# Performance work log

Measured on AMD Instinct MI355X. Metric: run time of the kernel, lower is better.

Reference implementation:

```python
import jax, jax.numpy as jnp
import numpy as np
from jax.ops import segment_sum

N = 100000
E = 3200000
IN_DIM = 256
OUT_DIM = 64
LN_EPS = 1e-5
NEG_SLOPE = 0.01


def setup_inputs() -> dict:
    key = jax.random.key(0)
    k1, k2, k3, k4, k5 = jax.random.split(key, 5)
    x = jax.random.normal(k1, (N, IN_DIM), dtype=jnp.float32)
    edge_index = jax.random.randint(k2, (2, E), 0, N, dtype=jnp.int32)
    edge_weight = jax.random.uniform(k3, (E,), dtype=jnp.float32)
    # GCNConv params (glorot-ish scale) + LayerNorm params
    W = jax.random.normal(k4, (IN_DIM, OUT_DIM), dtype=jnp.float32) / np.sqrt(IN_DIM)
    b = jnp.zeros((OUT_DIM,), dtype=jnp.float32)
    gamma = jnp.ones((OUT_DIM,), dtype=jnp.float32)
    beta = jnp.zeros((OUT_DIM,), dtype=jnp.float32)
    return {"x": x, "edge_index": edge_index, "edge_weight": edge_weight,
            "W": W, "b": b, "gamma": gamma, "beta": beta}


def _gcn_forward(x, edge_index, edge_weight, W, b, gamma, beta):
    n = x.shape[0]
    # add self-loops with weight 1 (PyG GCNConv default)
    loops = jnp.arange(n, dtype=edge_index.dtype)
    src = jnp.concatenate([edge_index[0], loops])   # [E+N] message sources
    dst = jnp.concatenate([edge_index[1], loops])   # [E+N] aggregation targets
    ew = jnp.concatenate([edge_weight, jnp.ones((n,), dtype=edge_weight.dtype)])
    # symmetric normalization: deg computed on dst via weighted scatter
    deg = segment_sum(ew, dst, num_segments=n)                   # [N]
    dinv = jnp.where(deg > 0, jax.lax.rsqrt(deg), 0.0)           # deg^{-1/2}
    norm = dinv[src] * ew * dinv[dst]                            # [E+N]
    h = x @ W                                                    # [N, OUT]
    agg = segment_sum(h[src] * norm[:, None], dst, num_segments=n)  # [N, OUT]
    y = agg + b
    # leaky_relu then LayerNorm over last dim
    y = jnp.where(y >= 0, y, NEG_SLOPE * y)
    mu = jnp.mean(y, axis=-1, keepdims=True)
    var = jnp.mean(jnp.square(y - mu), axis=-1, keepdims=True)
    return (y - mu) * jax.lax.rsqrt(var + LN_EPS) * gamma + beta


def reference(x, edge_index, edge_weight, W, b, gamma, beta):
    return _gcn_forward(x, edge_index, edge_weight, W, b, gamma, beta)
```

## Files before the change

### kernel.cpp

```cpp
#include <hip/hip_runtime.h>

#define NN 100000
#define NE 3200000
#define OVCAP 65536

#define BINSZ 64
#define NBIN ((NN + BINSZ - 1) / BINSZ)
#define NSEG 8
#define BINPAD 16
#define MAXPB 4096

struct OvEnt { int dst; int src; float ew; int pad; };


__global__ void k_zero(int* __restrict__ bincnt, int* __restrict__ ovcnt, int n) {
    int i = blockIdx.x * 256 + threadIdx.x;
    if (i < n) bincnt[i] = 0;
    if (i == 0) *ovcnt = 0;
}

__global__ void k_binscatter(const int* __restrict__ src, const int* __restrict__ dst,
                             const float* __restrict__ ew, int* __restrict__ bincnt,
                             uint2* __restrict__ binbuf, int segcap,
                             OvEnt* __restrict__ ov, int* __restrict__ ovcnt, int e) {
    int i = blockIdx.x * 256 + threadIdx.x;
    int seg = blockIdx.x & (NSEG - 1);
    if (i >= e) return;
    int s = src[i], d = dst[i];
    float w = ew[i];
    int cell = (d >> 6) * NSEG + seg;
    int pos = atomicAdd(&bincnt[cell * BINPAD], 1);
    if (pos < segcap) {
        unsigned key = (unsigned)s | ((unsigned)(d & 63) << 17);
        binbuf[(size_t)cell * segcap + pos] = make_uint2(key, __float_as_uint(w));
    } else {
        int op = atomicAdd(ovcnt, 1);
        if (op < OVCAP) { OvEnt t; t.dst = d; t.src = s; t.ew = w; t.pad = 0; ov[op] = t; }
    }
}

__global__ __launch_bounds__(256) void k_binsort(
    const int* __restrict__ bincnt, uint2* __restrict__ binbuf, int segcap,
    const OvEnt* __restrict__ ov, const int* __restrict__ ovcnt,
    float* __restrict__ dinv, int* __restrict__ off, int* __restrict__ ncnt,
    int* __restrict__ binov, int n) {
    __shared__ float sdeg[BINSZ];
    __shared__ int hcnt[BINSZ];
    __shared__ int hoff[BINSZ];
    __shared__ int spref[NSEG + 1];
    __shared__ int sov;
    __shared__ uint2 sbuf[MAXPB];
    int bin = blockIdx.x, t = threadIdx.x;
    if (t < BINSZ) { sdeg[t] = 0.f; hcnt[t] = 0; }
    if (t == 0) {
        int pref = 0, anyov = 0;
        for (int s2 = 0; s2 < NSEG; s2++) {
            int c = bincnt[(bin * NSEG + s2) * BINPAD];
            spref[s2] = pref;
            pref += (c < segcap ? c : segcap);
            if (c > segcap) anyov = 1;
        }
        spref[NSEG] = pref;
        sov = anyov;
        binov[bin] = anyov;
    }
    __syncthreads();
    int bc = spref[NSEG];
    uint2* base = binbuf + (size_t)bin * NSEG * segcap;
    for (int s2 = 0; s2 < NSEG; s2++) {
        int beg = spref[s2], len = spref[s2 + 1] - beg;
        const uint2* sp = base + (size_t)s2 * segcap;
        for (int j = t; j < len; j += 256) sbuf[beg + j] = sp[j];
    }
    __syncthreads();
    uint2 ent[16];
    int ne = 0;
#pragma unroll
    for (int p = 0; p < 16; p++) {
        int idx = t + p * 256;
        if (idx < bc) { ent[p] = sbuf[idx]; ne = p + 1; }
    }
#pragma unroll
    for (int p = 0; p < 16; p++) {
        if (p < ne) {
            int dl = (int)((ent[p].x >> 17) & 63u);
            atomicAdd(&hcnt[dl], 1);
            atomicAdd(&sdeg[dl], __uint_as_float(ent[p].y));
        }
    }
    if (sov) {
        int on = *ovcnt; if (on > OVCAP) on = OVCAP;
        for (int j = t; j < on; j += 256) {
            OvEnt e2 = ov[j];
            if ((e2.dst >> 6) == bin) atomicAdd(&sdeg[e2.dst & 63], e2.ew);
        }
    }
    __syncthreads();
    if (t < 64) {
        int v = hcnt[t];
        int inc = v;
#pragma unroll
        for (int o2 = 1; o2 < 64; o2 <<= 1) {
            int u = __shfl_up(inc, o2, 64);
            if (t >= o2) inc += u;
        }
        int excl = inc - v;
        hoff[t] = excl;
        int g = bin * BINSZ + t;
        if (g < n) {
            dinv[g] = rsqrtf(1.0f + sdeg[t]);
            off[g] = bin * NSEG * segcap + excl;
            ncnt[g] = v;
        }
    }
    __syncthreads();
#pragma unroll
    for (int p = 0; p < 16; p++) {
        if (p < ne) {
            int dl = (int)((ent[p].x >> 17) & 63u);
            int pos = atomicAdd(&hoff[dl], 1);
            sbuf[pos] = ent[p];
        }
    }
    __syncthreads();
    for (int j = t; j < bc; j += 256) base[j] = sbuf[j];
}

__global__ __launch_bounds__(256) void k_gather_s(
    const float* __restrict__ h, const float* __restrict__ dinv,
    const int* __restrict__ binov,
    const int* __restrict__ off, const int* __restrict__ ncnt,
    const uint2* __restrict__ sorted,
    const OvEnt* __restrict__ ov, const int* __restrict__ ovcnt,
    const float* __restrict__ bias, const float* __restrict__ gamma,
    const float* __restrict__ beta, float* __restrict__ out, int n) {
    int lane = threadIdx.x & 63, wid = threadIdx.x >> 6;
    int node = blockIdx.x * 4 + wid;
    if (node >= n) return;
    float di = dinv[node];
    float acc = h[(size_t)node * 64 + lane] * di * di;
    int beg = off[node], c0 = ncnt[node];
    for (int j = 0; j < c0; j += 64) {
        int c = c0 - j; if (c > 64) c = 64;
        int s = 0; float w = 0.f;
        if (lane < c) {
            uint2 v = sorted[beg + j + lane];
            s = (int)(v.x & 0x1FFFFu);
            w = __uint_as_float(v.y) * dinv[s] * di;
        }
        int i2 = 0;
        for (; i2 + 16 <= c; i2 += 16) {
            float hv[16], wv[16];
#pragma unroll
            for (int q = 0; q < 16; q++) {
                int si = __shfl(s, i2 + q, 64);
                wv[q] = __shfl(w, i2 + q, 64);
                hv[q] = h[(size_t)si * 64 + lane];
            }
#pragma unroll
            for (int q = 0; q < 16; q++) acc += hv[q] * wv[q];
        }
        if (i2 < c) {
            float hv[16], wv[16];
            int rem = c - i2;
#pragma unroll
            for (int q = 0; q < 16; q++) {
                if (q < rem) {
                    int si = __shfl(s, i2 + q, 64);
                    wv[q] = __shfl(w, i2 + q, 64);
                    hv[q] = h[(size_t)si * 64 + lane];
                } else { wv[q] = 0.f; hv[q] = 0.f; }
            }
#pragma unroll
            for (int q = 0; q < 16; q++) acc += hv[q] * wv[q];
        }
    }
    if (binov[node >> 6]) {
        int on = *ovcnt; if (on > OVCAP) on = OVCAP;
        for (int j = 0; j < on; j++) {
            OvEnt ent = ov[j];
            if (ent.dst == node)
                acc += h[(size_t)ent.src * 64 + lane] * dinv[ent.src] * ent.ew * di;
        }
    }
    float y = acc + bias[lane];
    y = (y >= 0.f) ? y : 0.01f * y;
    float sum = y;
#pragma unroll
    for (int o = 32; o > 0; o >>= 1) sum += __shfl_xor(sum, o, 64);
    float mu = sum * (1.0f / 64.0f);
    float d = y - mu;
    float v = d * d;
#pragma unroll
    for (int o = 32; o > 0; o >>= 1) v += __shfl_xor(v, o, 64);
    v *= (1.0f / 64.0f);
    out[(size_t)node * 64 + lane] = d * rsqrtf(v + 1e-5f) * gamma[lane] + beta[lane];
}

#define GR 64
#define GKC 32
#define XS_STRIDE 36
__global__ __launch_bounds__(256) void k_gemm(const float* __restrict__ x,
                                              const float* __restrict__ W,
                                              float* __restrict__ h, int n) {
    __shared__ float xs[GR][XS_STRIDE];
    __shared__ float wsh[GKC][64];
    int t = threadIdx.x;
    int tx = t & 15;
    int ty = t >> 4;
    int rbase = blockIdx.x * GR;
    float acc[4][4];
#pragma unroll
    for (int i = 0; i < 4; i++)
#pragma unroll
        for (int j = 0; j < 4; j++) acc[i][j] = 0.0f;

    for (int k0 = 0; k0 < 256; k0 += GKC) {
        const float4* wsrc = (const float4*)(W + k0 * 64);
        float4* wdst = (float4*)(&wsh[0][0]);
        wdst[t] = wsrc[t];
        wdst[t + 256] = wsrc[t + 256];
#pragma unroll
        for (int p = 0; p < 2; p++) {
            int f4 = p * 256 + t;
            int r = f4 >> 3;
            int kq = (f4 & 7) << 2;
            int row = rbase + r;
            float4 val = make_float4(0.f, 0.f, 0.f, 0.f);
            if (row < n) val = *(const float4*)(x + (size_t)row * 256 + k0 + kq);
            *(float4*)(&xs[r][kq]) = val;
        }
        __syncthreads();
        int r0 = ty * 4, c0 = tx * 4;
#pragma unroll
        for (int kk = 0; kk < GKC; kk += 4) {
            float4 wv[4];
#pragma unroll
            for (int m = 0; m < 4; m++) wv[m] = *(const float4*)(&wsh[kk + m][c0]);
#pragma unroll
            for (int i = 0; i < 4; i++) {
                float4 xv = *(const float4*)(&xs[r0 + i][kk]);
                acc[i][0] += xv.x * wv[0].x + xv.y * wv[1].x + xv.z * wv[2].x + xv.w * wv[3].x;
                acc[i][1] += xv.x * wv[0].y + xv.y * wv[1].y + xv.z * wv[2].y + xv.w * wv[3].y;
                acc[i][2] += xv.x * wv[0].z + xv.y * wv[1].z + xv.z * wv[2].z + xv.w * wv[3].z;
                acc[i][3] += xv.x * wv[0].w + xv.y * wv[1].w + xv.z * wv[2].w + xv.w * wv[3].w;
            }
        }
        __syncthreads();
    }
    int r0 = ty * 4, c0 = tx * 4;
#pragma unroll
    for (int i = 0; i < 4; i++) {
        int row = rbase + r0 + i;
        if (row < n) {
            float4 v = make_float4(acc[i][0], acc[i][1], acc[i][2], acc[i][3]);
            *(float4*)(h + (size_t)row * 64 + c0) = v;
        }
    }
}


__global__ void k_init(float* __restrict__ deg, int* __restrict__ cnt, int n) {
    int i = blockIdx.x * 256 + threadIdx.x;
    if (i < n) { deg[i] = 1.0f; cnt[i] = 0; }
}

__global__ void k_deg(const int* __restrict__ dst, const float* __restrict__ ew,
                      float* __restrict__ deg, int* __restrict__ cnt, int e) {
    int i = blockIdx.x * 256 + threadIdx.x;
    if (i < e) {
        int d = dst[i];
        atomicAdd(&deg[d], ew[i]);
        atomicAdd(&cnt[d], 1);
    }
}

#define SCAN_T 256
#define SCAN_E 8
__global__ void k_scan_blocks(const int* __restrict__ cnt, int* __restrict__ off,
                              int* __restrict__ bsum, int n) {
    __shared__ int sdata[SCAN_T];
    int base = blockIdx.x * (SCAN_T * SCAN_E);
    int t = threadIdx.x;
    int v[SCAN_E];
    int local = 0;
    int idx0 = base + t * SCAN_E;
#pragma unroll
    for (int i = 0; i < SCAN_E; i++) {
        int idx = idx0 + i;
        int c = (idx < n) ? cnt[idx] : 0;
        v[i] = local;
        local += c;
    }
    sdata[t] = local;
    __syncthreads();
    for (int o = 1; o < SCAN_T; o <<= 1) {
        int x = 0;
        if (t >= o) x = sdata[t - o];
        __syncthreads();
        sdata[t] += x;
        __syncthreads();
    }
    int excl = sdata[t] - local;
#pragma unroll
    for (int i = 0; i < SCAN_E; i++) {
        int idx = idx0 + i;
        if (idx < n) off[idx] = excl + v[i];
    }
    if (t == SCAN_T - 1) bsum[blockIdx.x] = sdata[t];
}

__global__ void k_scan_bsums(int* __restrict__ bsum, int nb) {
    int t = threadIdx.x;
    int v = (t < nb) ? bsum[t] : 0;
    int orig = v;
#pragma unroll
    for (int o = 1; o < 64; o <<= 1) {
        int u = __shfl_up(v, o, 64);
        if (t >= o) v += u;
    }
    if (t < nb) bsum[t] = v - orig;
}

__global__ void k_finalize(int* __restrict__ off, const int* __restrict__ bsum,
                           int* __restrict__ cursor, float* __restrict__ deg,
                           int n, int total) {
    int i = blockIdx.x * 256 + threadIdx.x;
    if (i < n) {
        int o = off[i] + bsum[i >> 11];
        off[i] = o;
        cursor[i] = o;
        deg[i] = rsqrtf(deg[i]);
    }
    if (i == 0) off[n] = total;
}

__global__ void k_scatter(const int* __restrict__ src, const int* __restrict__ dst,
                          const float* __restrict__ ew, const float* __restrict__ dinv,
                          int* __restrict__ cursor, int* __restrict__ ssrc,
                          float* __restrict__ snorm, int e) {
    int i = blockIdx.x * 256 + threadIdx.x;
    if (i < e) {
        int s = src[i], d = dst[i];
        float nm = dinv[s] * ew[i] * dinv[d];
        int pos = atomicAdd(&cursor[d], 1);
        ssrc[pos] = s;
        snorm[pos] = nm;
    }
}

__global__ __launch_bounds__(256) void k_gather(
    const float* __restrict__ h, const float* __restrict__ dinv,
    const int* __restrict__ off, const int* __restrict__ ssrc,
    const float* __restrict__ snorm, const float* __restrict__ bias,
    const float* __restrict__ gamma, const float* __restrict__ beta,
    float* __restrict__ out, int n) {
    int lane = threadIdx.x & 63;
    int wid = threadIdx.x >> 6;
    int node = blockIdx.x * 4 + wid;
    if (node >= n) return;
    float di = dinv[node];
    float acc = h[(size_t)node * 64 + lane] * di * di;
    int beg = off[node], end = off[node + 1];
    for (int j = beg; j < end; j += 64) {
        int cnt = end - j;
        if (cnt > 64) cnt = 64;
        int s = 0;
        float w = 0.f;
        if (lane < cnt) { s = ssrc[j + lane]; w = snorm[j + lane]; }
        for (int i2 = 0; i2 < cnt; i2++) {
            int si = __shfl(s, i2, 64);
            float wi = __shfl(w, i2, 64);
            acc += h[(size_t)si * 64 + lane] * wi;
        }
    }
    float y = acc + bias[lane];
    y = (y >= 0.f) ? y : 0.01f * y;
    float sum = y;
#pragma unroll
    for (int o = 32; o > 0; o >>= 1) sum += __shfl_xor(sum, o, 64);
    float mu = sum * (1.0f / 64.0f);
    float d = y - mu;
    float v = d * d;
#pragma unroll
    for (int o = 32; o > 0; o >>= 1) v += __shfl_xor(v, o, 64);
    v *= (1.0f / 64.0f);
    out[(size_t)node * 64 + lane] = d * rsqrtf(v + 1e-5f) * gamma[lane] + beta[lane];
}


extern "C" void kernel_launch(void* const* d_in, const int* in_sizes, int n_in,
                              void* d_out, int out_size, void* d_ws, size_t ws_size,
                              hipStream_t stream) {
    const float* x = (const float*)d_in[0];
    const int* ei = (const int*)d_in[1];
    const float* ew = (const float*)d_in[2];
    const float* W = (const float*)d_in[3];
    const float* b = (const float*)d_in[4];
    const float* gamma = (const float*)d_in[5];
    const float* beta = (const float*)d_in[6];
    float* out = (float*)d_out;

    const int n = NN, e = NE;
    const int* src = ei;
    const int* dst = ei + e;

    char* ws = (char*)d_ws;
    size_t o = 0;
    auto alloc = [&](size_t bytes) -> char* {
        char* r = ws + o;
        o = (o + bytes + 255) & ~(size_t)255;
        return r;
    };
    auto pad = [](size_t bytes) -> size_t { return (bytes + 255) & ~(size_t)255; };

    int nb_n = (n + 255) / 256;
    int nb_e = (e + 255) / 256;
    int nb_gemm = (n + GR - 1) / GR;
    int nb_w = (n + 3) / 4;

    size_t fixed = 0;
    fixed += pad((size_t)NBIN * NSEG * BINPAD * 4);
    fixed += 256;
    fixed += pad((size_t)OVCAP * 16);
    fixed += pad((size_t)n * 4);
    fixed += pad((size_t)n * 4);
    fixed += pad((size_t)n * 4);
    fixed += pad((size_t)NBIN * 4);
    fixed += pad((size_t)n * 64 * 4);

    int segcap = 0;
    if (ws_size >= fixed + pad((size_t)NBIN * NSEG * 512 * 8) + 1024) segcap = 512;
    else if (ws_size >= fixed + pad((size_t)NBIN * NSEG * 384 * 8) + 1024) segcap = 384;

    if (segcap > 0) {
        int* bincnt = (int*)alloc((size_t)NBIN * NSEG * BINPAD * 4);
        int* ovcnt = (int*)alloc(4);
        OvEnt* ov = (OvEnt*)alloc((size_t)OVCAP * 16);
        float* dinv = (float*)alloc((size_t)n * 4);
        int* off = (int*)alloc((size_t)n * 4);
        int* ncnt = (int*)alloc((size_t)n * 4);
        int* binov = (int*)alloc((size_t)NBIN * 4);
        float* h = (float*)alloc((size_t)n * 64 * 4);
        uint2* binbuf = (uint2*)alloc((size_t)NBIN * NSEG * segcap * 8);

        int nz = NBIN * NSEG * BINPAD;
        int nb_z = (nz + 255) / 256;
        k_zero<<<nb_z, 256, 0, stream>>>(bincnt, ovcnt, nz);
        k_binscatter<<<nb_e, 256, 0, stream>>>(src, dst, ew, bincnt, binbuf, segcap,
                                               ov, ovcnt, e);
        k_binsort<<<NBIN, 256, 0, stream>>>(bincnt, binbuf, segcap, ov, ovcnt,
                                            dinv, off, ncnt, binov, n);
        k_gemm<<<nb_gemm, 256, 0, stream>>>(x, W, h, n);
        k_gather_s<<<nb_w, 256, 0, stream>>>(h, dinv, binov, off, ncnt, binbuf,
                                             ov, ovcnt, b, gamma, beta, out, n);
    } else {
        float* deg = (float*)alloc((size_t)n * 4);
        int* cnt = (int*)alloc((size_t)n * 4);
        int* off = (int*)alloc((size_t)(n + 1) * 4);
        int* cursor = (int*)alloc((size_t)n * 4);
        int* bsum = (int*)alloc(64 * 4);
        float* h = (float*)alloc((size_t)n * 64 * 4);
        int* ssrc = (int*)alloc((size_t)e * 4);
        float* snorm = (float*)alloc((size_t)e * 4);
        int nb_scan = (n + SCAN_T * SCAN_E - 1) / (SCAN_T * SCAN_E);

        k_init<<<nb_n, 256, 0, stream>>>(deg, cnt, n);
        k_deg<<<nb_e, 256, 0, stream>>>(dst, ew, deg, cnt, e);
        k_scan_blocks<<<nb_scan, SCAN_T, 0, stream>>>(cnt, off, bsum, n);
        k_scan_bsums<<<1, 64, 0, stream>>>(bsum, nb_scan);
        k_finalize<<<nb_n, 256, 0, stream>>>(off, bsum, cursor, deg, n, e);
        k_scatter<<<nb_e, 256, 0, stream>>>(src, dst, ew, deg, cursor, ssrc, snorm, e);
        k_gemm<<<nb_gemm, 256, 0, stream>>>(x, W, h, n);
        k_gather<<<nb_w, 256, 0, stream>>>(h, deg, off, ssrc, snorm, b, gamma, beta, out, n);
    }
}
```

Measured before the change: 515.8 us.

## Replace per-edge global atomics with block-local histogram reservation in bin scatter

The scatter kernel now processes a contiguous chunk of edges per block, builds a shared-memory histogram over destination bins, and reserves space in each bin with one global atomic per bin per block. Edges then get their slots through shared atomics, which removes the per-edge global atomic and the 8-way segment split. The sort kernel reads a single contiguous bin region directly from global memory instead of gathering segments through LDS. In exchange each block reads the edge arrays twice and touches all ~1563 bin counters, and a contiguous bin buffer of 4096 slots per bin is assumed.

```diff
diff --git a/kernel.cpp b/kernel.cpp
--- a/kernel.cpp
+++ b/kernel.cpp
@@ -6,9 +6,8 @@
 
 #define BINSZ 64
 #define NBIN ((NN + BINSZ - 1) / BINSZ)
-#define NSEG 8
-#define BINPAD 16
 #define MAXPB 4096
+#define SCAT_BLOCKS 512
 
 struct OvEnt { int dst; int src; float ew; int pad; };
 
@@ -19,66 +18,68 @@
     if (i == 0) *ovcnt = 0;
 }
 
-__global__ void k_binscatter(const int* __restrict__ src, const int* __restrict__ dst,
-                             const float* __restrict__ ew, int* __restrict__ bincnt,
-                             uint2* __restrict__ binbuf, int segcap,
-                             OvEnt* __restrict__ ov, int* __restrict__ ovcnt, int e) {
-    int i = blockIdx.x * 256 + threadIdx.x;
-    int seg = blockIdx.x & (NSEG - 1);
-    if (i >= e) return;
-    int s = src[i], d = dst[i];
-    float w = ew[i];
-    int cell = (d >> 6) * NSEG + seg;
-    int pos = atomicAdd(&bincnt[cell * BINPAD], 1);
-    if (pos < segcap) {
-        unsigned key = (unsigned)s | ((unsigned)(d & 63) << 17);
-        binbuf[(size_t)cell * segcap + pos] = make_uint2(key, __float_as_uint(w));
-    } else {
-        int op = atomicAdd(ovcnt, 1);
-        if (op < OVCAP) { OvEnt t; t.dst = d; t.src = s; t.ew = w; t.pad = 0; ov[op] = t; }
+__global__ __launch_bounds__(256) void k_binscatter(
+    const int* __restrict__ src, const int* __restrict__ dst,
+    const float* __restrict__ ew, int* __restrict__ bincnt,
+    uint2* __restrict__ binbuf, int cap,
+    OvEnt* __restrict__ ov, int* __restrict__ ovcnt, int e) {
+    __shared__ int hist[NBIN];
+    int t = threadIdx.x;
+    int chunk = (e + gridDim.x - 1) / gridDim.x;
+    int beg = blockIdx.x * chunk;
+    int end = beg + chunk; if (end > e) end = e;
+    for (int j = t; j < NBIN; j += 256) hist[j] = 0;
+    __syncthreads();
+    for (int i = beg + t; i < end; i += 256)
+        atomicAdd(&hist[dst[i] >> 6], 1);
+    __syncthreads();
+    for (int j = t; j < NBIN; j += 256) {
+        int c = hist[j];
+        hist[j] = (c > 0) ? atomicAdd(&bincnt[j], c) : 0;
+    }
+    __syncthreads();
+    for (int i = beg + t; i < end; i += 256) {
+        int s = src[i], d = dst[i];
+        float w = ew[i];
+        int bin = d >> 6;
+        int pos = atomicAdd(&hist[bin], 1);
+        if (pos < cap) {
+            unsigned key = (unsigned)s | ((unsigned)(d & 63) << 17);
+            binbuf[(size_t)bin * cap + pos] = make_uint2(key, __float_as_uint(w));
+        } else {
+            int op = atomicAdd(ovcnt, 1);
+            if (op < OVCAP) { OvEnt t2; t2.dst = d; t2.src = s; t2.ew = w; t2.pad = 0; ov[op] = t2; }
+        }
     }
 }
 
 __global__ __launch_bounds__(256) void k_binsort(
-    const int* __restrict__ bincnt, uint2* __restrict__ binbuf, int segcap,
+    const int* __restrict__ bincnt, uint2* __restrict__ binbuf, int cap,
     const OvEnt* __restrict__ ov, const int* __restrict__ ovcnt,
     float* __restrict__ dinv, int* __restrict__ off, int* __restrict__ ncnt,
     int* __restrict__ binov, int n) {
     __shared__ float sdeg[BINSZ];
     __shared__ int hcnt[BINSZ];
     __shared__ int hoff[BINSZ];
-    __shared__ int spref[NSEG + 1];
     __shared__ int sov;
     __shared__ uint2 sbuf[MAXPB];
     int bin = blockIdx.x, t = threadIdx.x;
     if (t < BINSZ) { sdeg[t] = 0.f; hcnt[t] = 0; }
     if (t == 0) {
-        int pref = 0, anyov = 0;
-        for (int s2 = 0; s2 < NSEG; s2++) {
-            int c = bincnt[(bin * NSEG + s2) * BINPAD];
-            spref[s2] = pref;
-            pref += (c < segcap ? c : segcap);
-            if (c > segcap) anyov = 1;
-        }
-        spref[NSEG] = pref;
-        sov = anyov;
-        binov[bin] = anyov;
-    }
-    __syncthreads();
-    int bc = spref[NSEG];
-    uint2* base = binbuf + (size_t)bin * NSEG * segcap;
-    for (int s2 = 0; s2 < NSEG; s2++) {
-        int beg = spref[s2], len = spref[s2 + 1] - beg;
-        const uint2* sp = base + (size_t)s2 * segcap;
-        for (int j = t; j < len; j += 256) sbuf[beg + j] = sp[j];
-    }
-    __syncthreads();
+        int c = bincnt[bin];
+        sov = (c > cap);
+        binov[bin] = (c > cap);
+    }
+    __syncthreads();
+    int cnt = bincnt[bin];
+    int bc = cnt < cap ? cnt : cap;
+    uint2* base = binbuf + (size_t)bin * cap;
     uint2 ent[16];
     int ne = 0;
 #pragma unroll
     for (int p = 0; p < 16; p++) {
         int idx = t + p * 256;
-        if (idx < bc) { ent[p] = sbuf[idx]; ne = p + 1; }
+        if (idx < bc) { ent[p] = base[idx]; ne = p + 1; }
     }
 #pragma unroll
     for (int p = 0; p < 16; p++) {
@@ -109,7 +110,7 @@
         int g = bin * BINSZ + t;
         if (g < n) {
             dinv[g] = rsqrtf(1.0f + sdeg[t]);
-            off[g] = bin * NSEG * segcap + excl;
+            off[g] = bin * cap + excl;
             ncnt[g] = v;
         }
     }
@@ -420,7 +421,7 @@
     int nb_w = (n + 3) / 4;
 
     size_t fixed = 0;
-    fixed += pad((size_t)NBIN * NSEG * BINPAD * 4);
+    fixed += pad((size_t)NBIN * 4);
     fixed += 256;
     fixed += pad((size_t)OVCAP * 16);
     fixed += pad((size_t)n * 4);
@@ -429,12 +430,12 @@
     fixed += pad((size_t)NBIN * 4);
     fixed += pad((size_t)n * 64 * 4);
 
-    int segcap = 0;
-    if (ws_size >= fixed + pad((size_t)NBIN * NSEG * 512 * 8) + 1024) segcap = 512;
-    else if (ws_size >= fixed + pad((size_t)NBIN * NSEG * 384 * 8) + 1024) segcap = 384;
-
-    if (segcap > 0) {
-        int* bincnt = (int*)alloc((size_t)NBIN * NSEG * BINPAD * 4);
+    int cap = 0;
+    if (ws_size >= fixed + pad((size_t)NBIN * 4096 * 8) + 1024) cap = 4096;
+    else if (ws_size >= fixed + pad((size_t)NBIN * 3072 * 8) + 1024) cap = 3072;
+
+    if (cap > 0) {
+        int* bincnt = (int*)alloc((size_t)NBIN * 4);
         int* ovcnt = (int*)alloc(4);
         OvEnt* ov = (OvEnt*)alloc((size_t)OVCAP * 16);
         float* dinv = (float*)alloc((size_t)n * 4);
@@ -442,14 +443,13 @@
         int* ncnt = (int*)alloc((size_t)n * 4);
         int* binov = (int*)alloc((size_t)NBIN * 4);
         float* h = (float*)alloc((size_t)n * 64 * 4);
-        uint2* binbuf = (uint2*)alloc((size_t)NBIN * NSEG * segcap * 8);
-
-        int nz = NBIN * NSEG * BINPAD;
-        int nb_z = (nz + 255) / 256;
-        k_zero<<<nb_z, 256, 0, stream>>>(bincnt, ovcnt, nz);
-        k_binscatter<<<nb_e, 256, 0, stream>>>(src, dst, ew, bincnt, binbuf, segcap,
-                                               ov, ovcnt, e);
-        k_binsort<<<NBIN, 256, 0, stream>>>(bincnt, binbuf, segcap, ov, ovcnt,
+        uint2* binbuf = (uint2*)alloc((size_t)NBIN * cap * 8);
+
+        int nb_z = (NBIN + 255) / 256;
+        k_zero<<<nb_z, 256, 0, stream>>>(bincnt, ovcnt, NBIN);
+        k_binscatter<<<SCAT_BLOCKS, 256, 0, stream>>>(src, dst, ew, bincnt, binbuf, cap,
+                                                      ov, ovcnt, e);
+        k_binsort<<<NBIN, 256, 0, stream>>>(bincnt, binbuf, cap, ov, ovcnt,
                                             dinv, off, ncnt, binov, n);
         k_gemm<<<nb_gemm, 256, 0, stream>>>(x, W, h, n);
         k_gather_s<<<nb_w, 256, 0, stream>>>(h, dinv, binov, off, ncnt, binbuf,
```

New measurement: 470.8 us. 1.1x faster.
